# Kernel optimization log

Measured on AMD Instinct MI355X. Metric: run time of the kernel, lower is better.

Reference implementation:

```python
import jax, jax.numpy as jnp
import numpy as np

N, C, H, W = 4, 256, 64, 64
S = 2          # scale_factor
K = 5          # up_kernel
G = 1          # up_group
CK = 64        # compressed_channels


def conv2d(x, w, b, pad):
    out = jax.lax.conv_general_dilated(
        x, w, window_strides=(1, 1), padding=[(pad, pad), (pad, pad)],
        dimension_numbers=('NCHW', 'OIHW', 'NCHW'))
    return out + b[None, :, None, None]


def pixel_shuffle(x, r):
    n, cr, h, w = x.shape
    c = cr // (r * r)
    return x.reshape(n, c, r, r, h, w).transpose(0, 1, 4, 2, 5, 3).reshape(n, c, h * r, w * r)


def grid_sample_border(img, grid):
    # img [N,C,Hi,Wi], grid [N,Ho,Wo,2] in [-1,1] (x,y); bilinear, border pad, align_corners=True
    n, c, hi, wi = img.shape
    gx = (grid[..., 0] + 1.0) * 0.5 * (wi - 1)
    gy = (grid[..., 1] + 1.0) * 0.5 * (hi - 1)
    gx = jnp.clip(gx, 0.0, wi - 1.0)
    gy = jnp.clip(gy, 0.0, hi - 1.0)
    x0 = jnp.floor(gx).astype(jnp.int32)
    y0 = jnp.floor(gy).astype(jnp.int32)
    x1 = jnp.minimum(x0 + 1, wi - 1)
    y1 = jnp.minimum(y0 + 1, hi - 1)
    wx = (gx - x0)[..., None]
    wy = (gy - y0)[..., None]
    bidx = jnp.arange(n)[:, None, None]
    def gather(yy, xx):
        return img[bidx, :, yy, xx]  # [N,Ho,Wo,C]
    v00 = gather(y0, x0)
    v01 = gather(y0, x1)
    v10 = gather(y1, x0)
    v11 = gather(y1, x1)
    out = (v00 * (1 - wx) * (1 - wy) + v01 * wx * (1 - wy)
           + v10 * (1 - wx) * wy + v11 * wx * wy)
    return out.transpose(0, 3, 1, 2)


def carafe2(features, masks, k, g, up):
    n, c, h, w = features.shape
    cg = c // g
    k2 = k * k
    # masks [N, g*k2, h*up, w*up] -> per-pixel kernels [n,g,h,w,k2,up2]
    m = masks.reshape(n, g, k2, h, up, w, up)
    m = m.transpose(0, 1, 2, 3, 5, 4, 6).reshape(n, g, k2, h, w, up * up)
    kern = m.transpose(0, 1, 3, 4, 2, 5)            # [n,g,h,w,k2,up2]
    f = features.reshape(n, g, cg, h, w)
    p = k // 2
    fp = jnp.pad(f, ((0, 0), (0, 0), (0, 0), (p, p), (p, p)))
    patches = jnp.stack([fp[:, :, :, i:i + h, j:j + w]
                         for i in range(k) for j in range(k)], axis=-1)  # [n,g,cg,h,w,k2]
    xp = patches.transpose(0, 1, 3, 4, 2, 5)        # [n,g,h,w,cg,k2]
    out = jnp.einsum('nghwck,nghwku->nghwcu', xp, kern)  # [n,g,h,w,cg,up2]
    out = out.transpose(0, 1, 4, 2, 3, 5).reshape(n, c * up * up, h, w)
    return pixel_shuffle(out, up)


def setup_inputs() -> dict:
    key = jax.random.key(0)
    ks = jax.random.split(key, 4)
    x = jax.random.normal(ks[0], (N, C, H, W), dtype=jnp.float32)
    w_comp = jax.random.normal(ks[1], (CK, C, 1, 1), dtype=jnp.float32) * 0.05
    b_comp = jnp.zeros((CK,), dtype=jnp.float32)
    w_ker = jax.random.normal(ks[2], (G * K * K, CK, 3, 3), dtype=jnp.float32) * 0.001
    b_ker = jnp.zeros((G * K * K,), dtype=jnp.float32)
    w_off = jax.random.normal(ks[3], (G * 2 * S * S, CK, 3, 3), dtype=jnp.float32) * 0.01
    b_off = jnp.zeros((G * 2 * S * S,), dtype=jnp.float32)
    return {'x': x, 'w_comp': w_comp, 'b_comp': b_comp,
            'w_ker': w_ker, 'b_ker': b_ker, 'w_off': w_off, 'b_off': b_off}


def reference(x, w_comp, b_comp, w_ker, b_ker, w_off, b_off):
    cx = conv2d(x, w_comp, b_comp, 0)               # channel compressor (1x1)
    offset = conv2d(cx, w_off, b_off, 1)            # [N, 2*S*S, H, W]
    mask = conv2d(cx, w_ker, b_ker, 1)              # [N, G*K*K, H, W]
    # kernel_space_normalizer: softmax over the K*K kernel positions
    n, mc, h, w = mask.shape
    mask = jax.nn.softmax(mask.reshape(n, mc // (K * K), K * K, h, w), axis=2)
    mask = mask.reshape(n, mc, h, w)
    # kernel_space_expander
    off = pixel_shuffle(offset, S).transpose(0, 2, 3, 1)  # [N, H*S, W*S, 2]
    off = off * jnp.array([2.0 / (w - 1), 2.0 / (h - 1)], dtype=off.dtype)
    gh = jnp.repeat(jnp.linspace(-1.0, 1.0, h), S)  # [H*S]
    gw = jnp.repeat(jnp.linspace(-1.0, 1.0, w), S)  # [W*S]
    base = jnp.stack(jnp.broadcast_arrays(gw[None, :], gh[:, None]), axis=-1)  # [H*S, W*S, 2]
    grid = base[None] + off
    mask_ = grid_sample_border(mask, grid)          # [N, G*K*K, H*S, W*S]
    return carafe2(x, mask_, K, G, S)
```

## Files before the change

kernel.cpp:

```cpp
#include <hip/hip_runtime.h>
#include <math.h>

#define NB 4
#define C_IN 256
#define CKC 64
#define HWSZ 4096
#define K2 25
#define NOC2 40

#define WS_CX    0
#define WS_OFF   (WS_CX + NB*CKC*HWSZ)
#define WS_MASK  (WS_OFF + NB*8*HWSZ)
#define WS_WT    (WS_MASK + NB*K2*HWSZ)

#define NWT (CKC * 9 * NOC2)
#define NWC (C_IN * CKC)

__global__ void k_wt(const float* __restrict__ wk, const float* __restrict__ wo,
                     const float* __restrict__ wc,
                     float* __restrict__ wT, float* __restrict__ wcT) {
  int i = blockIdx.x * 256 + threadIdx.x;
  if (i < NWT) {
    int oc = i % NOC2;
    int r = i / NOC2;
    int tap = r % 9, c = r / 9;
    float v = 0.f;
    if (oc < 8)       v = wo[(oc * CKC + c) * 9 + tap];
    else if (oc < 33) v = wk[((oc - 8) * CKC + c) * 9 + tap];
    wT[i] = v;
  } else {
    int j = i - NWT;
    if (j < NWC) {
      int c = j >> 6, ck = j & 63;
      wcT[j] = wc[ck * C_IN + c];
    }
  }
}

__global__ __launch_bounds__(512) void k_cs(const float* __restrict__ x,
    const float* __restrict__ wcT, const float* __restrict__ bc,
    const float* __restrict__ wT, const float* __restrict__ bk, const float* __restrict__ bo,
    float* __restrict__ offb, float* __restrict__ maskb) {
  __shared__ float s_x[64 * 108];
  __shared__ float s_tile[64 * 108];
  float* s_res = s_x;

  int t = threadIdx.x;
  int n = blockIdx.y;
  int tile = blockIdx.x;
  int x0 = (tile & 3) * 16, y0 = (tile >> 2) * 4;
  const float* xn = x + (size_t)n * (C_IN * HWSZ);

  int srcOff[14];
  unsigned vb = 0, wb = 0;
  #pragma unroll
  for (int it = 0; it < 14; it++) {
    int idx = t + it * 512;
    int c = idx / 108;
    int rem = idx - c * 108;
    int row = rem / 18, col = rem - row * 18;
    int gy = y0 - 1 + row, gx = x0 - 1 + col;
    bool wr = (idx < 6912);
    bool ok = wr & ((unsigned)gy < 64u) & ((unsigned)gx < 64u);
    srcOff[it] = ok ? (c * HWSZ + gy * 64 + gx) : 0;
    vb |= (ok ? 1u : 0u) << it;
    wb |= (wr ? 1u : 0u) << it;
  }
  float rv[14];
  #pragma unroll
  for (int it = 0; it < 14; it++) rv[it] = xn[srcOff[it]];

  int p = t & 63;
  int g = __builtin_amdgcn_readfirstlane(t >> 6);
  int pos1 = p + 64;
  int pos1c = (pos1 < 108) ? pos1 : 107;
  float a0[8], a1[8];
  #pragma unroll
  for (int i = 0; i < 8; i++) { a0[i] = bc[g * 8 + i]; a1[i] = a0[i]; }

  for (int cc = 0; cc < 4; cc++) {
    __syncthreads();
    #pragma unroll
    for (int it = 0; it < 14; it++)
      if (wb & (1u << it)) s_x[t + it * 512] = (vb & (1u << it)) ? rv[it] : 0.f;
    __syncthreads();
    if (cc < 3) {
      const float* xb = xn + (size_t)(cc + 1) * 64 * HWSZ;
      #pragma unroll
      for (int it = 0; it < 14; it++) rv[it] = xb[srcOff[it]];
    }
    const float* wbase = wcT + (cc * 64) * 64 + g * 8;
    #pragma unroll 4
    for (int c = 0; c < 64; c++) {
      float v0 = s_x[c * 108 + p];
      float v1 = s_x[c * 108 + pos1c];
      const float* w = wbase + c * 64;
      #pragma unroll
      for (int i = 0; i < 8; i++) { a0[i] += v0 * w[i]; a1[i] += v1 * w[i]; }
    }
  }
  #pragma unroll
  for (int i = 0; i < 8; i++) s_tile[(g * 8 + i) * 108 + p] = a0[i];
  if (pos1 < 108) {
    #pragma unroll
    for (int i = 0; i < 8; i++) s_tile[(g * 8 + i) * 108 + pos1] = a1[i];
  }
  __syncthreads();

  int px = p & 15, py = p >> 4;
  float acc[5];
  #pragma unroll
  for (int j = 0; j < 5; j++) acc[j] = 0.f;
  const float* wg = wT + g * 5;
  const float* tl0 = s_tile + py * 18 + px;

#define LOADWIN(dst, cidx)                                   \
  {                                                          \
    const float* tlc = tl0 + (cidx) * 108;                   \
    _Pragma("unroll")                                        \
    for (int tap = 0; tap < 9; tap++) {                      \
      int dy = tap / 3, dx = tap % 3;                        \
      dst[tap] = tlc[dy * 18 + dx];                          \
    }                                                        \
  }
#define FMAWIN(src, cidx)                                    \
  {                                                          \
    const float* wc9 = wg + (cidx) * 9 * NOC2;               \
    _Pragma("unroll")                                        \
    for (int tap = 0; tap < 9; tap++) {                      \
      float v = src[tap];                                    \
      const float* w = wc9 + tap * NOC2;                     \
      _Pragma("unroll")                                      \
      for (int j = 0; j < 5; j++) acc[j] += v * w[j];        \
    }                                                        \
  }

  float wa[9], wbuf[9];
  LOADWIN(wa, 0)
  LOADWIN(wbuf, 1)
  #pragma unroll 1
  for (int c = 0; c < CKC; c += 2) {
    FMAWIN(wa, c)
    if (c + 2 < CKC) LOADWIN(wa, c + 2)
    FMAWIN(wbuf, c + 1)
    if (c + 3 < CKC) LOADWIN(wbuf, c + 3)
  }
#undef LOADWIN
#undef FMAWIN

  #pragma unroll
  for (int j = 0; j < 5; j++) s_res[(g * 5 + j) * 64 + p] = acc[j];
  __syncthreads();

  int hw = (y0 + py) * 64 + x0 + px;
  offb[(n * 8 + g) * HWSZ + hw] = s_res[g * 64 + p] + bo[g];
  if (t < 64) {
    float m[25], mx = -1e30f;
    #pragma unroll
    for (int k = 0; k < 25; k++) { m[k] = s_res[(8 + k) * 64 + p] + bk[k]; mx = fmaxf(mx, m[k]); }
    float s = 0.f;
    #pragma unroll
    for (int k = 0; k < 25; k++) { m[k] = __expf(m[k] - mx); s += m[k]; }
    float inv = 1.f / s;
    #pragma unroll
    for (int k = 0; k < 25; k++) maskb[(n * 25 + k) * HWSZ + hw] = m[k] * inv;
  }
}

__global__ __launch_bounds__(256, 4) void k_carafe(const float* __restrict__ x,
    const float* __restrict__ offb, const float* __restrict__ maskb,
    float* __restrict__ out) {
  __attribute__((aligned(16))) __shared__ float s_patch[32 * 202];
  __attribute__((aligned(16))) __shared__ float s_kern[32 * 25 * 4];
  int t = threadIdx.x;
  int b = blockIdx.x;
  int n = b >> 8;
  int r = b & 255;
  int half = r & 1;
  int wq = (r >> 1) & 3;
  int aa = r >> 3;
  int a = aa + (aa & 16);
  int yout = (a & 15) * 8 + wq * 2 + ((a >> 5) & 1);
  int w0 = wq * 16;
  int cbase = n * C_IN + half * 128;

  int srcOff[13];
  int dstOff[13];
  unsigned vbits = 0;
  unsigned wbits = 0;
  #pragma unroll
  for (int it = 0; it < 13; it++) {
    int e = t + it * 256;
    int c = e / 100;
    int rem = e - c * 100;
    int rg = rem / 10;
    int c2 = rem - rg * 10;
    int row = (rg < 5) ? (a - 2 + rg) : (a + 9 + rg);
    int gc0 = w0 - 2 + c2 * 2;
    bool wr = (e < 3200);
    bool ok = wr & ((unsigned)row < 64u) & ((unsigned)gc0 < 64u);
    srcOff[it] = ok ? (c * HWSZ + row * 64 + gc0) : 0;
    dstOff[it] = wr ? 2 * (e + c) : 0;
    vbits |= (ok ? 1u : 0u) << it;
    wbits |= (wr ? 1u : 0u) << it;
  }

  float2 rv[13];
  {
    const float* xn = x + (size_t)cbase * HWSZ;
    #pragma unroll
    for (int it = 0; it < 13; it++) rv[it] = *(const float2*)(xn + srcOff[it]);
  }

  if (t < 128) {
    int p = t >> 2, u = t & 3;
    int hb = p >> 4, wl = p & 15;
    int h = a + hb * 16;
    int wcol = w0 + wl;
    float ox = offb[(n * 8 + u) * HWSZ + h * 64 + wcol];
    float oy = offb[(n * 8 + 4 + u) * HWSZ + h * 64 + wcol];
    float gx = fminf(fmaxf((float)wcol + ox, 0.f), 63.f);
    float gy = fminf(fmaxf((float)h + oy, 0.f), 63.f);
    float fx0 = floorf(gx), fy0 = floorf(gy);
    int x0 = (int)fx0, y0 = (int)fy0;
    float fx = gx - fx0, fy = gy - fy0;
    int x1 = min(x0 + 1, 63), y1 = min(y0 + 1, 63);
    float w11 = fx * fy;
    float w10 = fy - w11, w01 = fx - w11, w00 = 1.f - fx - fy + w11;
    const float* mb = maskb + n * (K2 * HWSZ);
    int i00 = y0 * 64 + x0, i01 = y0 * 64 + x1;
    int i10 = y1 * 64 + x0, i11 = y1 * 64 + x1;
    #pragma unroll 5
    for (int k = 0; k < 25; k++) {
      const float* mk = mb + k * HWSZ;
      float v = w00 * mk[i00] + w01 * mk[i01] + w10 * mk[i10] + w11 * mk[i11];
      s_kern[(p * 25 + k) * 4 + u] = v;
    }
  }

  int cl = t & 31, g = t >> 5;
  int hb = g >> 2, wl0 = (g & 3) * 4;
  float* s_out = s_patch;

  for (int cc = 0; cc < 4; cc++) {
    __syncthreads();
    #pragma unroll
    for (int it = 0; it < 13; it++) {
      if (wbits & (1u << it)) {
        float2 v = (vbits & (1u << it)) ? rv[it] : make_float2(0.f, 0.f);
        *(float2*)(&s_patch[dstOff[it]]) = v;
      }
    }
    __syncthreads();
    if (cc < 3) {
      const float* xn = x + (size_t)(cbase + (cc + 1) * 32) * HWSZ;
      #pragma unroll
      for (int it = 0; it < 13; it++) rv[it] = *(const float2*)(xn + srcOff[it]);
    }
    float acc[4][4];
    #pragma unroll
    for (int i = 0; i < 4; i++)
      acc[i][0] = acc[i][1] = acc[i][2] = acc[i][3] = 0.f;
    const float* pc = s_patch + cl * 202 + hb * 100 + wl0;
    #pragma unroll
    for (int dy = 0; dy < 5; dy++) {
      float r8[8];
      #pragma unroll
      for (int j = 0; j < 8; j++) r8[j] = pc[dy * 20 + j];
      #pragma unroll
      for (int pr = 0; pr < 4; pr++) {
        const float4* kp = (const float4*)(s_kern + (((g * 4 + pr) * 25) + dy * 5) * 4);
        #pragma unroll
        for (int dx = 0; dx < 5; dx++) {
          float f = r8[pr + dx];
          float4 k4 = kp[dx];
          acc[pr][0] += f * k4.x;
          acc[pr][1] += f * k4.y;
          acc[pr][2] += f * k4.z;
          acc[pr][3] += f * k4.w;
        }
      }
    }
    __syncthreads();
    #pragma unroll
    for (int pr = 0; pr < 4; pr++) {
      int wl = wl0 + pr;
      #pragma unroll
      for (int u = 0; u < 4; u++) {
        int xo = wl * 8 + u * 2 + hb;
        s_out[cl * 130 + xo] = acc[pr][u];
      }
    }
    __syncthreads();
    float* obase = out + ((size_t)(cbase + cc * 32) * 128 + yout) * 128;
    #pragma unroll
    for (int it = 0; it < 4; it++) {
      int q2 = t + it * 256;
      int rowc = q2 >> 5;
      int col4 = q2 & 31;
      const float* sp = s_out + rowc * 130 + col4 * 4;
      float4 v = make_float4(sp[0], sp[1], sp[2], sp[3]);
      *(float4*)(obase + (size_t)rowc * (128 * 128) + col4 * 4) = v;
    }
  }
}

extern "C" void kernel_launch(void* const* d_in, const int* in_sizes, int n_in,
                              void* d_out, int out_size, void* d_ws, size_t ws_size,
                              hipStream_t stream) {
  const float* x      = (const float*)d_in[0];
  const float* w_comp = (const float*)d_in[1];
  const float* b_comp = (const float*)d_in[2];
  const float* w_ker  = (const float*)d_in[3];
  const float* b_ker  = (const float*)d_in[4];
  const float* w_off  = (const float*)d_in[5];
  const float* b_off  = (const float*)d_in[6];
  float* out = (float*)d_out;
  float* ws = (float*)d_ws;
  float* offb  = ws + WS_OFF;
  float* maskb = ws + WS_MASK;
  float* wT    = ws + WS_WT;
  float* wcT   = ws + WS_CX;

  hipLaunchKernelGGL(k_wt, dim3((NWT + NWC + 255) / 256), dim3(256), 0, stream,
                     w_ker, w_off, w_comp, wT, wcT);
  hipLaunchKernelGGL(k_cs, dim3(64, 4), dim3(512), 0, stream,
                     x, wcT, b_comp, wT, b_ker, b_off, offb, maskb);
  hipLaunchKernelGGL(k_carafe, dim3(1024), dim3(256), 0, stream, x, offb, maskb, out);
}
```

Before: 184.6 us.

## Double-buffer input staging in 32-channel chunks with float2 loads

Replaces the single 64-channel shared staging buffer with two 32-channel buffers that are swapped each iteration, so the next chunk is written while the current one is consumed, leaving one barrier per chunk instead of two. Global loads become float2 vector loads over a padded 20-wide row layout (columns x0-2 .. x0+17), which cuts the number of load instructions and the registers held for staging. The cost is twice as many chunk iterations and extra index arithmetic for the padded offsets. Out-of-range pairs are zero-filled as whole float2 elements.

```diff
diff --git a/kernel.cpp b/kernel.cpp
--- a/kernel.cpp
+++ b/kernel.cpp
@@ -41,9 +41,10 @@
     const float* __restrict__ wcT, const float* __restrict__ bc,
     const float* __restrict__ wT, const float* __restrict__ bk, const float* __restrict__ bo,
     float* __restrict__ offb, float* __restrict__ maskb) {
-  __shared__ float s_x[64 * 108];
-  __shared__ float s_tile[64 * 108];
-  float* s_res = s_x;
+  __attribute__((aligned(16))) __shared__ float s_xa[32 * 120];
+  __attribute__((aligned(16))) __shared__ float s_xb[32 * 120];
+  __attribute__((aligned(16))) __shared__ float s_tile[64 * 108];
+  float* s_res = s_xa;
 
   int t = threadIdx.x;
   int n = blockIdx.y;
@@ -51,54 +52,77 @@
   int x0 = (tile & 3) * 16, y0 = (tile >> 2) * 4;
   const float* xn = x + (size_t)n * (C_IN * HWSZ);
 
-  int srcOff[14];
-  unsigned vb = 0, wb = 0;
-  #pragma unroll
-  for (int it = 0; it < 14; it++) {
-    int idx = t + it * 512;
-    int c = idx / 108;
-    int rem = idx - c * 108;
-    int row = rem / 18, col = rem - row * 18;
-    int gy = y0 - 1 + row, gx = x0 - 1 + col;
-    bool wr = (idx < 6912);
-    bool ok = wr & ((unsigned)gy < 64u) & ((unsigned)gx < 64u);
-    srcOff[it] = ok ? (c * HWSZ + gy * 64 + gx) : 0;
-    vb |= (ok ? 1u : 0u) << it;
-    wb |= (wr ? 1u : 0u) << it;
-  }
-  float rv[14];
-  #pragma unroll
-  for (int it = 0; it < 14; it++) rv[it] = xn[srcOff[it]];
+  int srcOff[4];
+  unsigned vbits = 0, wbits = 0;
+  #pragma unroll
+  for (int it = 0; it < 4; it++) {
+    int e = t + it * 512;
+    int c = e / 60;
+    int rem = e - c * 60;
+    int row = rem / 10, pr = rem - row * 10;
+    int gy = y0 - 1 + row;
+    int gc0 = x0 - 2 + pr * 2;
+    bool wr = (e < 1920);
+    bool ok = wr & ((unsigned)gy < 64u) & ((unsigned)gc0 < 63u);
+    srcOff[it] = ok ? (c * HWSZ + gy * 64 + gc0) : 0;
+    vbits |= (ok ? 1u : 0u) << it;
+    wbits |= (wr ? 1u : 0u) << it;
+  }
+
+  float2 rv[4];
+  #pragma unroll
+  for (int it = 0; it < 4; it++) rv[it] = *(const float2*)(xn + srcOff[it]);
 
   int p = t & 63;
   int g = __builtin_amdgcn_readfirstlane(t >> 6);
   int pos1 = p + 64;
   int pos1c = (pos1 < 108) ? pos1 : 107;
+  int poff0 = (p / 18) * 20 + (p % 18) + 1;
+  int poff1 = (pos1c / 18) * 20 + (pos1c % 18) + 1;
   float a0[8], a1[8];
   #pragma unroll
   for (int i = 0; i < 8; i++) { a0[i] = bc[g * 8 + i]; a1[i] = a0[i]; }
 
-  for (int cc = 0; cc < 4; cc++) {
-    __syncthreads();
-    #pragma unroll
-    for (int it = 0; it < 14; it++)
-      if (wb & (1u << it)) s_x[t + it * 512] = (vb & (1u << it)) ? rv[it] : 0.f;
-    __syncthreads();
-    if (cc < 3) {
-      const float* xb = xn + (size_t)(cc + 1) * 64 * HWSZ;
-      #pragma unroll
-      for (int it = 0; it < 14; it++) rv[it] = xb[srcOff[it]];
-    }
-    const float* wbase = wcT + (cc * 64) * 64 + g * 8;
+  float* sA = s_xa;
+  float* sB = s_xb;
+  #pragma unroll
+  for (int it = 0; it < 4; it++)
+    if (wbits & (1u << it))
+      *(float2*)(&sA[2 * t + it * 1024]) =
+          (vbits & (1u << it)) ? rv[it] : make_float2(0.f, 0.f);
+  {
+    const float* xb = xn + (size_t)32 * HWSZ;
+    #pragma unroll
+    for (int it = 0; it < 4; it++) rv[it] = *(const float2*)(xb + srcOff[it]);
+  }
+  __syncthreads();
+
+  for (int hc = 0; hc < 8; hc++) {
+    if (hc < 7) {
+      #pragma unroll
+      for (int it = 0; it < 4; it++)
+        if (wbits & (1u << it))
+          *(float2*)(&sB[2 * t + it * 1024]) =
+              (vbits & (1u << it)) ? rv[it] : make_float2(0.f, 0.f);
+    }
+    if (hc < 6) {
+      const float* xb = xn + (size_t)(hc + 2) * 32 * HWSZ;
+      #pragma unroll
+      for (int it = 0; it < 4; it++) rv[it] = *(const float2*)(xb + srcOff[it]);
+    }
+    const float* wbase = wcT + (hc * 32) * 64 + g * 8;
     #pragma unroll 4
-    for (int c = 0; c < 64; c++) {
-      float v0 = s_x[c * 108 + p];
-      float v1 = s_x[c * 108 + pos1c];
+    for (int c = 0; c < 32; c++) {
+      float v0 = sA[c * 120 + poff0];
+      float v1 = sA[c * 120 + poff1];
       const float* w = wbase + c * 64;
       #pragma unroll
       for (int i = 0; i < 8; i++) { a0[i] += v0 * w[i]; a1[i] += v1 * w[i]; }
     }
-  }
+    __syncthreads();
+    float* tmp = sA; sA = sB; sB = tmp;
+  }
+
   #pragma unroll
   for (int i = 0; i < 8; i++) s_tile[(g * 8 + i) * 108 + p] = a0[i];
   if (pos1 < 108) {
```

Result: no change. 182.1 us (-1.4%).
